# Kernel tuning notes

Measured on AMD Instinct MI355X. Metric: run time of the kernel, lower is better.

Reference implementation:

```python
import jax, jax.numpy as jnp
import numpy as np

WS = 8        # window_size
NH = 8        # num_heads
LN_EPS = 1e-5

# static relative-position index table [WS*WS, WS*WS], values in [0, (2*WS-1)**2)
def _rel_index(ws):
    coords = np.arange(ws)
    grid = np.stack(np.meshgrid(coords, coords, indexing='ij')).reshape(2, -1)  # [2, W2]
    rel = grid[:, :, None] - grid[:, None, :]            # [2, W2, W2]
    rel = rel.transpose(1, 2, 0).copy()                   # [W2, W2, 2]
    rel[..., 0] += ws - 1
    rel[..., 1] += ws - 1
    rel[..., 0] *= 2 * ws - 1
    return rel.sum(-1)                                    # [W2, W2]

REL_IDX = jnp.asarray(_rel_index(WS))


def _ln(x):
    # LayerNorm without affine params (elementwise_affine=False)
    mu = jnp.mean(x, axis=-1, keepdims=True)
    var = jnp.var(x, axis=-1, keepdims=True)
    return (x - mu) * jax.lax.rsqrt(var + LN_EPS)


def setup_inputs() -> dict:
    key = jax.random.key(0)
    ks = jax.random.split(key, 16)
    B, Hg, Wg, C = 8, 64, 64, 256
    L = Hg * Wg
    s = 0.02
    inp = {
        'x': jax.random.normal(ks[0], (B, L, C), jnp.float32),
        't_embed': jax.random.normal(ks[1], (B, C), jnp.float32),
        'H': Hg,
        'W': Wg,
        'adaln1_w': s * jax.random.normal(ks[2], (C, 2 * C), jnp.float32),
        'adaln1_b': jnp.zeros((2 * C,), jnp.float32),
        'adaln2_w': s * jax.random.normal(ks[3], (C, 2 * C), jnp.float32),
        'adaln2_b': jnp.zeros((2 * C,), jnp.float32),
        'bias_table': s * jax.random.normal(ks[4], ((2 * WS - 1) ** 2, NH), jnp.float32),
        'q_w': s * jax.random.normal(ks[5], (C, C), jnp.float32),
        'q_b': jnp.zeros((C,), jnp.float32),
        'k_w': s * jax.random.normal(ks[6], (C, C), jnp.float32),
        'k_b': jnp.zeros((C,), jnp.float32),
        'v_w': s * jax.random.normal(ks[7], (C, C), jnp.float32),
        'v_b': jnp.zeros((C,), jnp.float32),
        'o_w': s * jax.random.normal(ks[8], (C, C), jnp.float32),
        'o_b': jnp.zeros((C,), jnp.float32),
        'ffn1_w': s * jax.random.normal(ks[9], (C, 4 * C), jnp.float32),
        'ffn1_b': jnp.zeros((4 * C,), jnp.float32),
        'ffn2_w': s * jax.random.normal(ks[10], (4 * C, C), jnp.float32),
        'ffn2_b': jnp.zeros((C,), jnp.float32),
    }
    return inp


def reference(x, t_embed, H, W, adaln1_w, adaln1_b, adaln2_w, adaln2_b,
              bias_table, q_w, q_b, k_w, k_b, v_w, v_b, o_w, o_b,
              ffn1_w, ffn1_b, ffn2_w, ffn2_b):
    B, L, C = x.shape
    d = C // NH
    W2 = WS * WS
    sh = WS // 2  # cyclic shift (shifted=True)

    # --- AdaLN1 ---
    ss = t_embed @ adaln1_w + adaln1_b              # [B, 2C]
    scale, shift = jnp.split(ss, 2, axis=-1)
    xn = _ln(x) * (1.0 + scale[:, None, :]) + shift[:, None, :]

    # --- shifted window partition ---
    xg = xn.reshape(B, H, W, C)
    xg = jnp.roll(xg, (-sh, -sh), axis=(1, 2))
    xw = xg.reshape(B, H // WS, WS, W // WS, WS, C).transpose(0, 1, 3, 2, 4, 5)
    xw = xw.reshape(-1, W2, C)                       # [nwB, W2, C]
    nwB = xw.shape[0]

    # --- window attention with relative position bias ---
    q = (xw @ q_w + q_b).reshape(nwB, W2, NH, d).transpose(0, 2, 1, 3)
    k = (xw @ k_w + k_b).reshape(nwB, W2, NH, d).transpose(0, 2, 1, 3)
    v = (xw @ v_w + v_b).reshape(nwB, W2, NH, d).transpose(0, 2, 1, 3)
    logits = jnp.einsum('whqd,whkd->whqk', q, k) * (d ** -0.5)
    bias = bias_table[REL_IDX.reshape(-1)].reshape(W2, W2, NH).transpose(2, 0, 1)
    logits = logits + bias[None].astype(logits.dtype)
    attn = jax.nn.softmax(logits, axis=-1)
    out = jnp.einsum('whqk,whkd->whqd', attn, v).transpose(0, 2, 1, 3).reshape(nwB, W2, C)
    out = out @ o_w + o_b

    # --- window reverse + unshift ---
    xm = out.reshape(B, H // WS, W // WS, WS, WS, C).transpose(0, 1, 3, 2, 4, 5)
    xm = xm.reshape(B, H, W, C)
    xm = jnp.roll(xm, (sh, sh), axis=(1, 2))
    x = x + xm.reshape(B, L, C)

    # --- AdaLN2 + FFN (GELU exact, matching torch nn.GELU) ---
    ss2 = t_embed @ adaln2_w + adaln2_b
    sc2, sh2 = jnp.split(ss2, 2, axis=-1)
    xn2 = _ln(x) * (1.0 + sc2[:, None, :]) + sh2[:, None, :]
    h = jax.nn.gelu(xn2 @ ffn1_w + ffn1_b, approximate=False)
    x = x + (h @ ffn2_w + ffn2_b)
    return x
```

## Files before the change

### kernel.cpp

```cpp
#include <hip/hip_runtime.h>
#include <math.h>

#define WS_ 8
#define NH_ 8
#define C_ 256
#define B_ 8
#define M_ 32768
#define SH_ 4
#define LN_EPS 1e-5f
#define SL_ 8388608

typedef __attribute__((ext_vector_type(8))) short bf16x8;
typedef __attribute__((ext_vector_type(4))) float f32x4;

__device__ inline float b2f(unsigned short u) {
    union { unsigned int i; float f; } c; c.i = ((unsigned int)u) << 16; return c.f;
}
__device__ inline unsigned short f2b(float f) {
    union { unsigned int i; float f; } c; c.f = f;
    unsigned int u = c.i;
    return (unsigned short)((u + 0x7FFFu + ((u >> 16) & 1u)) >> 16);
}
__device__ inline float gelu_f(float x) {
    float t = 1.59576912160573f * (x + 0.044715f * x * x * x);
    return x / (1.f + __expf(-t));
}

__global__ void prep_k(const float* __restrict__ qw, const float* __restrict__ kw,
                       const float* __restrict__ vw, const float* __restrict__ ow,
                       const float* __restrict__ f1w, const float* __restrict__ f2w,
                       const float* __restrict__ qb, const float* __restrict__ kb,
                       const float* __restrict__ vb, const float* __restrict__ bt,
                       const float* __restrict__ te,
                       const float* __restrict__ a1w, const float* __restrict__ a1b,
                       const float* __restrict__ a2w, const float* __restrict__ a2b,
                       unsigned short* __restrict__ qkvT, unsigned short* __restrict__ oT,
                       unsigned short* __restrict__ f1T, unsigned short* __restrict__ f2T,
                       float* __restrict__ qkvB, float* __restrict__ bias_full,
                       float* __restrict__ ss1, float* __restrict__ ss2) {
    int t = blockIdx.x * 256 + threadIdx.x;
    if (t < 196608) {
        int n = t >> 8, k = t & 255;
        const float* w = n < 256 ? qw : (n < 512 ? kw : vw);
        qkvT[t] = f2b(w[k * 256 + (n & 255)]);
    } else if (t < 262144) {
        int i = t - 196608; int n = i >> 8, k = i & 255;
        oT[i] = f2b(ow[k * 256 + n]);
    } else if (t < 524288) {
        int i = t - 262144; int n = i >> 8, k = i & 255;
        f1T[i] = f2b(f1w[k * 1024 + n]);
    } else if (t < 786432) {
        int i = t - 524288; int n = i >> 10, k = i & 1023;
        f2T[i] = f2b(f2w[k * 256 + n]);
    } else if (t < 787200) {
        int i = t - 786432;
        qkvB[i] = i < 256 ? qb[i] : (i < 512 ? kb[i - 256] : vb[i - 512]);
    } else if (t < 819968) {
        int i = t - 787200;
        int head = i >> 12, qk = i & 4095;
        int q = qk >> 6, k = qk & 63;
        int qh = q >> 3, qw2 = q & 7, kh = k >> 3, kw2 = k & 7;
        bias_full[i] = bt[((qh - kh + 7) * 15 + (qw2 - kw2 + 7)) * 8 + head];
    } else if (t < 828160) {
        int i = t - 819968;
        int which = i >> 12;
        int rem = i & 4095;
        int b = rem >> 9, col = rem & 511;
        const float* w = which ? a2w : a1w;
        const float* bb = which ? a2b : a1b;
        const float* tr = te + b * C_;
        float acc = bb[col];
        for (int k = 0; k < C_; ++k) acc += tr[k] * w[k * 512 + col];
        (which ? ss2 : ss1)[b * 512 + col] = acc;
    }
}

__global__ __launch_bounds__(256) void ln_win_k(const float* __restrict__ x,
                                                const float* __restrict__ ss,
                                                unsigned short* __restrict__ xw) {
    int t = blockIdx.x * 4 + (threadIdx.x >> 6);
    int lane = threadIdx.x & 63;
    int b = t >> 12, rem = t & 4095;
    int hg = rem >> 6, wg = rem & 63;
    int hs = (hg + SH_) & 63, wsrc = (wg + SH_) & 63;
    size_t src = ((size_t)b << 12) + (hs << 6) + wsrc;
    float4 v = *(const float4*)&x[src * C_ + lane * 4];
    float s = v.x + v.y + v.z + v.w;
    float s2 = v.x * v.x + v.y * v.y + v.z * v.z + v.w * v.w;
#pragma unroll
    for (int m = 1; m < 64; m <<= 1) { s += __shfl_xor(s, m); s2 += __shfl_xor(s2, m); }
    float mu = s * (1.f / 256.f);
    float rstd = rsqrtf(s2 * (1.f / 256.f) - mu * mu + LN_EPS);
    float4 sc = *(const float4*)&ss[b * 512 + lane * 4];
    float4 sh = *(const float4*)&ss[b * 512 + 256 + lane * 4];
    int win = (b << 6) + ((hg >> 3) << 3) + (wg >> 3);
    int pos = ((hg & 7) << 3) + (wg & 7);
    ushort4 pk;
    pk.x = f2b((v.x - mu) * rstd * (1.f + sc.x) + sh.x);
    pk.y = f2b((v.y - mu) * rstd * (1.f + sc.y) + sh.y);
    pk.z = f2b((v.z - mu) * rstd * (1.f + sc.z) + sh.z);
    pk.w = f2b((v.w - mu) * rstd * (1.f + sc.w) + sh.w);
    *(ushort4*)(xw + (size_t)(win * 64 + pos) * C_ + lane * 4) = pk;
}

template <int KDIM, int MODE, int NT, int MINW>
__global__ __launch_bounds__(256, MINW) void gemm_bf16_k(
    const unsigned short* __restrict__ A, const unsigned short* __restrict__ Bt,
    const float* __restrict__ bias, const float* __restrict__ res,
    void* __restrict__ Cout, int Nout) {
    __shared__ __align__(16) unsigned short As[4][128 * 32];
    __shared__ __align__(16) unsigned short Bs[4][128 * 32];
    const int blk = blockIdx.x;
    const int xcd = blk & 7;
    const int idx = blk >> 3;
    const int mt = xcd + ((idx / NT) << 3);
    const int nt = idx % NT;
    const int bm = mt * 128, bn = nt * 128;
    const int tid = threadIdx.x;
    const int w = tid >> 6, lane = tid & 63;
    const int quad = lane >> 4, l16 = lane & 15;
    const int wm = (w >> 1) * 64, wn = (w & 1) * 64;
    const int srow = lane >> 2;
    const int qlog = ((lane & 3) ^ ((lane >> 3) & 3)) << 3;
    const int rsw = ((l16 >> 1) & 3) << 3;

    f32x4 acc[4][4] = {};

    for (int k0 = 0; k0 < KDIM; k0 += 128) {
        if (k0) __syncthreads();
#pragma unroll
        for (int h = 0; h < 4; ++h) {
#pragma unroll
            for (int j = 0; j < 2; ++j) {
                int r = j * 64 + w * 16 + srow;
                const unsigned short* ga = A + (size_t)(bm + r) * KDIM + k0 + h * 32 + qlog;
                unsigned short* la = &As[h][j * 2048 + w * 512 + lane * 8];
                __builtin_amdgcn_global_load_lds(
                    (const __attribute__((address_space(1))) void*)ga,
                    (__attribute__((address_space(3))) void*)la, 16, 0, 0);
                const unsigned short* gb = Bt + (size_t)(bn + r) * KDIM + k0 + h * 32 + qlog;
                unsigned short* lb = &Bs[h][j * 2048 + w * 512 + lane * 8];
                __builtin_amdgcn_global_load_lds(
                    (const __attribute__((address_space(1))) void*)gb,
                    (__attribute__((address_space(3))) void*)lb, 16, 0, 0);
            }
        }
        __syncthreads();
#pragma unroll
        for (int h = 0; h < 4; ++h) {
            bf16x8 af[4], bfr[4];
#pragma unroll
            for (int i = 0; i < 4; ++i)
                af[i] = *(const bf16x8*)&As[h][(wm + i * 16 + l16) * 32 + ((quad << 3) ^ rsw)];
#pragma unroll
            for (int j = 0; j < 4; ++j)
                bfr[j] = *(const bf16x8*)&Bs[h][(wn + j * 16 + l16) * 32 + ((quad << 3) ^ rsw)];
#pragma unroll
            for (int i = 0; i < 4; ++i)
#pragma unroll
                for (int j = 0; j < 4; ++j)
                    acc[i][j] = __builtin_amdgcn_mfma_f32_16x16x32_bf16(
                        bfr[j], af[i], acc[i][j], 0, 0, 0);
        }
    }

#pragma unroll
    for (int i = 0; i < 4; ++i) {
        const int row = bm + wm + i * 16 + l16;
        size_t rowbase = 0;
        if (MODE == 0) {
            int win = row >> 6, pos = row & 63;
            rowbase = (size_t)win * 16384 + pos * 32;
        } else {
            rowbase = (size_t)row * Nout;
        }
#pragma unroll
        for (int j = 0; j < 4; ++j) {
            const int col = bn + wn + j * 16 + quad * 4;
            float4 bv = *(const float4*)&bias[col];
            float v0 = acc[i][j][0] + bv.x, v1 = acc[i][j][1] + bv.y;
            float v2 = acc[i][j][2] + bv.z, v3 = acc[i][j][3] + bv.w;
            if (MODE == 0) {
                int which = col >> 8, head = (col >> 5) & 7, dc = col & 31;
                ushort4 pk = {f2b(v0), f2b(v1), f2b(v2), f2b(v3)};
                *(ushort4*)((unsigned short*)Cout + (size_t)which * SL_ + rowbase +
                            head * 2048 + dc) = pk;
            } else if (MODE == 2) {
                ushort4 pk = {f2b(gelu_f(v0)), f2b(gelu_f(v1)),
                              f2b(gelu_f(v2)), f2b(gelu_f(v3))};
                *(ushort4*)((unsigned short*)Cout + rowbase + col) = pk;
            } else {
                float4 rv = *(const float4*)&res[rowbase + col];
                float4 ov = {v0 + rv.x, v1 + rv.y, v2 + rv.z, v3 + rv.w};
                *(float4*)&((float*)Cout)[rowbase + col] = ov;
            }
        }
    }
}

__global__ __launch_bounds__(512, 2) void oproj_ln_k(
    const unsigned short* __restrict__ A, const unsigned short* __restrict__ Bt,
    const float* __restrict__ bias, const float* __restrict__ res,
    float* __restrict__ x1, const float* __restrict__ ss2,
    unsigned short* __restrict__ xn2) {
    __shared__ __align__(16) unsigned short As[4][128 * 32];
    __shared__ __align__(16) unsigned short Bs[4][256 * 32];
    const int bm = blockIdx.x * 128;
    const int tid = threadIdx.x;
    const int w = tid >> 6, lane = tid & 63;
    const int quad = lane >> 4, l16 = lane & 15;
    const int wrow = (w >> 2) * 64, wcol = (w & 3) * 64;
    const int rsw = ((l16 >> 1) & 3) << 3;
    const int srow = tid >> 2;
    const int gch = ((tid & 3) ^ ((srow >> 1) & 3)) << 3;

    f32x4 acc[4][4] = {};

    for (int k0 = 0; k0 < 256; k0 += 128) {
        if (k0) __syncthreads();
#pragma unroll
        for (int h = 0; h < 4; ++h) {
            const unsigned short* ga = A + (size_t)(bm + srow) * 256 + k0 + h * 32 + gch;
            __builtin_amdgcn_global_load_lds(
                (const __attribute__((address_space(1))) void*)ga,
                (__attribute__((address_space(3))) void*)&As[h][tid * 8], 16, 0, 0);
#pragma unroll
            for (int s = 0; s < 2; ++s) {
                const unsigned short* gb = Bt + (size_t)(s * 128 + srow) * 256 + k0 + h * 32 + gch;
                __builtin_amdgcn_global_load_lds(
                    (const __attribute__((address_space(1))) void*)gb,
                    (__attribute__((address_space(3))) void*)&Bs[h][s * 4096 + tid * 8], 16, 0, 0);
            }
        }
        __syncthreads();
#pragma unroll
        for (int h = 0; h < 4; ++h) {
            bf16x8 af[4], bfr[4];
#pragma unroll
            for (int i = 0; i < 4; ++i)
                af[i] = *(const bf16x8*)&As[h][(wrow + i * 16 + l16) * 32 + ((quad << 3) ^ rsw)];
#pragma unroll
            for (int j = 0; j < 4; ++j)
                bfr[j] = *(const bf16x8*)&Bs[h][(wcol + j * 16 + l16) * 32 + ((quad << 3) ^ rsw)];
#pragma unroll
            for (int i = 0; i < 4; ++i)
#pragma unroll
                for (int j = 0; j < 4; ++j)
                    acc[i][j] = __builtin_amdgcn_mfma_f32_16x16x32_bf16(
                        bfr[j], af[i], acc[i][j], 0, 0, 0);
        }
    }

    float ps[4], ps2[4];
#pragma unroll
    for (int i = 0; i < 4; ++i) {
        const int row = bm + wrow + i * 16 + l16;
        int win = row >> 6, pos = row & 63;
        int b = win >> 6, wh = (win >> 3) & 7, ww = win & 7;
        int hg = (wh << 3) + (pos >> 3), wg = (ww << 3) + (pos & 7);
        int hd = (hg + SH_) & 63, wd = (wg + SH_) & 63;
        size_t rowbase = (((size_t)b << 12) + (hd << 6) + wd) * C_;
        float s = 0.f, s2 = 0.f;
#pragma unroll
        for (int j = 0; j < 4; ++j) {
            const int col = wcol + j * 16 + quad * 4;
            float4 bv = *(const float4*)&bias[col];
            float4 rv = *(const float4*)&res[rowbase + col];
            float4 ov = {acc[i][j][0] + bv.x + rv.x, acc[i][j][1] + bv.y + rv.y,
                         acc[i][j][2] + bv.z + rv.z, acc[i][j][3] + bv.w + rv.w};
            *(float4*)&x1[rowbase + col] = ov;
            acc[i][j][0] = ov.x; acc[i][j][1] = ov.y;
            acc[i][j][2] = ov.z; acc[i][j][3] = ov.w;
            s += ov.x + ov.y + ov.z + ov.w;
            s2 += ov.x * ov.x + ov.y * ov.y + ov.z * ov.z + ov.w * ov.w;
        }
        ps[i] = s; ps2[i] = s2;
    }
#pragma unroll
    for (int i = 0; i < 4; ++i) {
        ps[i] += __shfl_xor(ps[i], 16);  ps[i] += __shfl_xor(ps[i], 32);
        ps2[i] += __shfl_xor(ps2[i], 16); ps2[i] += __shfl_xor(ps2[i], 32);
    }
    float* sred = (float*)&As[0][0];
    __syncthreads();
    if (quad == 0) {
#pragma unroll
        for (int i = 0; i < 4; ++i) {
            int r = i * 16 + l16;
            sred[(w * 64 + r) * 2 + 0] = ps[i];
            sred[(w * 64 + r) * 2 + 1] = ps2[i];
        }
    }
    __syncthreads();
#pragma unroll
    for (int i = 0; i < 4; ++i) {
        int r = i * 16 + l16;
        float s = 0.f, s2 = 0.f;
#pragma unroll
        for (int cw = 0; cw < 4; ++cw) {
            s  += sred[(((w >> 2) * 4 + cw) * 64 + r) * 2 + 0];
            s2 += sred[(((w >> 2) * 4 + cw) * 64 + r) * 2 + 1];
        }
        float mu = s * (1.f / 256.f);
        float rstd = rsqrtf(s2 * (1.f / 256.f) - mu * mu + LN_EPS);
        const int row = bm + wrow + i * 16 + l16;
        int win = row >> 6, pos = row & 63;
        int b = win >> 6, wh = (win >> 3) & 7, ww = win & 7;
        int hg = (wh << 3) + (pos >> 3), wg = (ww << 3) + (pos & 7);
        int hd = (hg + SH_) & 63, wd = (wg + SH_) & 63;
        size_t rowbase = (((size_t)b << 12) + (hd << 6) + wd) * C_;
#pragma unroll
        for (int j = 0; j < 4; ++j) {
            const int col = wcol + j * 16 + quad * 4;
            float4 scv = *(const float4*)&ss2[b * 512 + col];
            float4 shv = *(const float4*)&ss2[b * 512 + 256 + col];
            ushort4 pk;
            pk.x = f2b((acc[i][j][0] - mu) * rstd * (1.f + scv.x) + shv.x);
            pk.y = f2b((acc[i][j][1] - mu) * rstd * (1.f + scv.y) + shv.y);
            pk.z = f2b((acc[i][j][2] - mu) * rstd * (1.f + scv.z) + shv.z);
            pk.w = f2b((acc[i][j][3] - mu) * rstd * (1.f + scv.w) + shv.w);
            *(ushort4*)(xn2 + rowbase + col) = pk;
        }
    }
}

__global__ __launch_bounds__(256) void attn_mfma_k(
    const unsigned short* __restrict__ qkv, const float* __restrict__ bias_full,
    unsigned short* __restrict__ attn_out) {
    __shared__ __align__(16) unsigned short Pb[4][64 * 66];
    __shared__ __align__(16) unsigned short Vt[4][32 * 66];
    const int w = threadIdx.x >> 6, lane = threadIdx.x & 63;
    const int wh = blockIdx.x * 4 + w;
    const int win = wh >> 3, head = wh & 7;
    const int quad = lane >> 4, l16 = lane & 15;

    const unsigned short* qp = qkv + (size_t)win * 16384 + head * 2048;
    const unsigned short* kp = qp + SL_;
    const unsigned short* vp = qp + 2 * (size_t)SL_;

    {
        const uint4* v4 = (const uint4*)(vp + lane * 32);
        unsigned short* dst = &Vt[w][0];
#pragma unroll
        for (int c = 0; c < 4; ++c) {
            uint4 u = v4[c];
            unsigned int uu[4] = {u.x, u.y, u.z, u.w};
#pragma unroll
            for (int p = 0; p < 4; ++p) {
                int d0 = c * 8 + p * 2;
                dst[d0 * 66 + lane] = (unsigned short)(uu[p] & 0xffff);
                dst[(d0 + 1) * 66 + lane] = (unsigned short)(uu[p] >> 16);
            }
        }
    }

    bf16x8 qf[4], kf[4];
#pragma unroll
    for (int i = 0; i < 4; ++i) {
        qf[i] = *(const bf16x8*)(qp + (i * 16 + l16) * 32 + quad * 8);
        kf[i] = *(const bf16x8*)(kp + (i * 16 + l16) * 32 + quad * 8);
    }

    f32x4 s[4][4] = {};
#pragma unroll
    for (int i = 0; i < 4; ++i)
#pragma unroll
        for (int j = 0; j < 4; ++j)
            s[i][j] = __builtin_amdgcn_mfma_f32_16x16x32_bf16(qf[i], kf[j], s[i][j], 0, 0, 0);

    const float scale = 0.17677669529663687f;
    const float* bf = bias_full + head * 4096;
    float rs[4][4];
#pragma unroll
    for (int i = 0; i < 4; ++i) {
#pragma unroll
        for (int r = 0; r < 4; ++r) {
            int row = i * 16 + quad * 4 + r;
            float acc = 0.f;
#pragma unroll
            for (int j = 0; j < 4; ++j) {
                float e = __expf(s[i][j][r] * scale + bf[row * 64 + j * 16 + l16]);
                s[i][j][r] = e;
                acc += e;
            }
#pragma unroll
            for (int msk = 1; msk < 16; msk <<= 1) acc += __shfl_xor(acc, msk);
            rs[i][r] = 1.f / acc;
        }
    }

#pragma unroll
    for (int i = 0; i < 4; ++i)
#pragma unroll
        for (int j = 0; j < 4; ++j)
#pragma unroll
            for (int r = 0; r < 4; ++r)
                Pb[w][(i * 16 + quad * 4 + r) * 66 + j * 16 + l16] = f2b(s[i][j][r]);

    __syncthreads();

    f32x4 o[4][2] = {};
#pragma unroll
    for (int st = 0; st < 2; ++st) {
        bf16x8 bv[2];
#pragma unroll
        for (int jo = 0; jo < 2; ++jo)
            bv[jo] = *(const bf16x8*)&Vt[w][(jo * 16 + l16) * 66 + st * 32 + quad * 8];
#pragma unroll
        for (int i = 0; i < 4; ++i) {
            bf16x8 af = *(const bf16x8*)&Pb[w][(i * 16 + l16) * 66 + st * 32 + quad * 8];
#pragma unroll
            for (int jo = 0; jo < 2; ++jo)
                o[i][jo] = __builtin_amdgcn_mfma_f32_16x16x32_bf16(af, bv[jo], o[i][jo], 0, 0, 0);
        }
    }

#pragma unroll
    for (int i = 0; i < 4; ++i)
#pragma unroll
        for (int jo = 0; jo < 2; ++jo)
#pragma unroll
            for (int r = 0; r < 4; ++r) {
                int row = i * 16 + quad * 4 + r;
                int d = jo * 16 + l16;
                attn_out[((size_t)(win * 64 + row)) * C_ + head * 32 + d] =
                    f2b(o[i][jo][r] * rs[i][r]);
            }
}

extern "C" void kernel_launch(void* const* d_in, const int* in_sizes, int n_in,
                              void* d_out, int out_size, void* d_ws, size_t ws_size,
                              hipStream_t stream) {
    const float* x        = (const float*)d_in[0];
    const float* t_embed  = (const float*)d_in[1];
    const float* adaln1_w = (const float*)d_in[4];
    const float* adaln1_b = (const float*)d_in[5];
    const float* adaln2_w = (const float*)d_in[6];
    const float* adaln2_b = (const float*)d_in[7];
    const float* bt       = (const float*)d_in[8];
    const float* q_w = (const float*)d_in[9],  *q_b = (const float*)d_in[10];
    const float* k_w = (const float*)d_in[11], *k_b = (const float*)d_in[12];
    const float* v_w = (const float*)d_in[13], *v_b = (const float*)d_in[14];
    const float* o_w = (const float*)d_in[15], *o_b = (const float*)d_in[16];
    const float* f1_w = (const float*)d_in[17], *f1_b = (const float*)d_in[18];
    const float* f2_w = (const float*)d_in[19], *f2_b = (const float*)d_in[20];
    float* out = (float*)d_out;

    char* wsb = (char*)d_ws;
    float* ss1            = (float*)(wsb + 0);
    float* ss2            = (float*)(wsb + 16384);
    float* qkvB           = (float*)(wsb + 32768);
    unsigned short* qkvT  = (unsigned short*)(wsb + 36864);
    unsigned short* oT    = (unsigned short*)(wsb + 430080);
    unsigned short* f1T   = (unsigned short*)(wsb + 561152);
    unsigned short* f2T   = (unsigned short*)(wsb + 1085440);
    float* bias_full      = (float*)(wsb + 1609728);
    unsigned short* xw    = (unsigned short*)(wsb + 2097152);
    unsigned short* qkv   = (unsigned short*)(wsb + 18874368);
    unsigned short* attn  = (unsigned short*)(wsb + 69206016);
    unsigned short* xn2   = xw;
    unsigned short* hbuf  = qkv;
    float* x1             = (float*)(wsb + 85983232);

    prep_k<<<3235, 256, 0, stream>>>(q_w, k_w, v_w, o_w, f1_w, f2_w, q_b, k_b, v_b, bt,
                                     t_embed, adaln1_w, adaln1_b, adaln2_w, adaln2_b,
                                     qkvT, oT, f1T, f2T, qkvB, bias_full, ss1, ss2);
    ln_win_k<<<8192, 256, 0, stream>>>(x, ss1, xw);

    gemm_bf16_k<256, 0, 6, 2><<<1536, 256, 0, stream>>>(xw, qkvT, qkvB, nullptr, qkv, 768);

    attn_mfma_k<<<1024, 256, 0, stream>>>(qkv, bias_full, attn);

    oproj_ln_k<<<256, 512, 0, stream>>>(attn, oT, o_b, x, x1, ss2, xn2);

    gemm_bf16_k<256, 2, 8, 2><<<2048, 256, 0, stream>>>(xn2, f1T, f1_b, nullptr, hbuf, 1024);
    gemm_bf16_k<1024, 3, 2, 2><<<512, 256, 0, stream>>>(hbuf, f2T, f2_b, x1, out, 256);
}
```

Measured before the change: 270.8 us.

## Halve GEMM K-step LDS footprint and stage bf16 epilogue through swizzled LDS

The generic bf16 GEMM now loads 64-wide K chunks instead of 128, halving shared memory to 32KB so more blocks can be resident. Launch-bound minimum waves change to 3 for the QKV and FFN1 GEMMs and to 1 for FFN2. For the bf16-output modes (QKV scatter and GELU), the epilogue writes results into swizzled LDS and then emits full 16-byte row-contiguous stores instead of scattered 8-byte stores. The cost is twice as many barriers in the K loop and an extra LDS round trip in the epilogue.

```diff
diff --git a/kernel.cpp b/kernel.cpp
--- a/kernel.cpp
+++ b/kernel.cpp
@@ -108,8 +108,9 @@
     const unsigned short* __restrict__ A, const unsigned short* __restrict__ Bt,
     const float* __restrict__ bias, const float* __restrict__ res,
     void* __restrict__ Cout, int Nout) {
-    __shared__ __align__(16) unsigned short As[4][128 * 32];
-    __shared__ __align__(16) unsigned short Bs[4][128 * 32];
+    __shared__ __align__(16) unsigned short smem[16384];
+    unsigned short (*As)[4096] = (unsigned short (*)[4096])&smem[0];
+    unsigned short (*Bs)[4096] = (unsigned short (*)[4096])&smem[8192];
     const int blk = blockIdx.x;
     const int xcd = blk & 7;
     const int idx = blk >> 3;
@@ -126,10 +127,10 @@
 
     f32x4 acc[4][4] = {};
 
-    for (int k0 = 0; k0 < KDIM; k0 += 128) {
+    for (int k0 = 0; k0 < KDIM; k0 += 64) {
         if (k0) __syncthreads();
 #pragma unroll
-        for (int h = 0; h < 4; ++h) {
+        for (int h = 0; h < 2; ++h) {
 #pragma unroll
             for (int j = 0; j < 2; ++j) {
                 int r = j * 64 + w * 16 + srow;
@@ -147,7 +148,7 @@
         }
         __syncthreads();
 #pragma unroll
-        for (int h = 0; h < 4; ++h) {
+        for (int h = 0; h < 2; ++h) {
             bf16x8 af[4], bfr[4];
 #pragma unroll
             for (int i = 0; i < 4; ++i)
@@ -164,32 +165,56 @@
         }
     }
 
-#pragma unroll
-    for (int i = 0; i < 4; ++i) {
-        const int row = bm + wm + i * 16 + l16;
-        size_t rowbase = 0;
-        if (MODE == 0) {
-            int win = row >> 6, pos = row & 63;
-            rowbase = (size_t)win * 16384 + pos * 32;
-        } else {
-            rowbase = (size_t)row * Nout;
-        }
-#pragma unroll
-        for (int j = 0; j < 4; ++j) {
-            const int col = bn + wn + j * 16 + quad * 4;
-            float4 bv = *(const float4*)&bias[col];
-            float v0 = acc[i][j][0] + bv.x, v1 = acc[i][j][1] + bv.y;
-            float v2 = acc[i][j][2] + bv.z, v3 = acc[i][j][3] + bv.w;
-            if (MODE == 0) {
+    if constexpr (MODE == 0 || MODE == 2) {
+        __syncthreads();
+#pragma unroll
+        for (int i = 0; i < 4; ++i) {
+            const int lrow = wm + i * 16 + l16;
+#pragma unroll
+            for (int j = 0; j < 4; ++j) {
+                const int lcol = wn + j * 16 + quad * 4;
+                float4 bv = *(const float4*)&bias[bn + lcol];
+                float v0 = acc[i][j][0] + bv.x, v1 = acc[i][j][1] + bv.y;
+                float v2 = acc[i][j][2] + bv.z, v3 = acc[i][j][3] + bv.w;
+                ushort4 pk;
+                if (MODE == 2) {
+                    pk.x = f2b(gelu_f(v0)); pk.y = f2b(gelu_f(v1));
+                    pk.z = f2b(gelu_f(v2)); pk.w = f2b(gelu_f(v3));
+                } else {
+                    pk.x = f2b(v0); pk.y = f2b(v1); pk.z = f2b(v2); pk.w = f2b(v3);
+                }
+                int sw = (lcol >> 3) ^ (lrow & 7);
+                *(ushort4*)&smem[lrow * 128 + sw * 8 + (lcol & 7)] = pk;
+            }
+        }
+        __syncthreads();
+#pragma unroll
+        for (int p = 0; p < 8; ++p) {
+            const int lrow = p * 16 + (tid >> 4);
+            const int c16 = tid & 15;
+            bf16x8 v = *(const bf16x8*)&smem[lrow * 128 + ((c16 ^ (lrow & 7)) * 8)];
+            const int grow = bm + lrow;
+            if (MODE == 2) {
+                *(bf16x8*)((unsigned short*)Cout + (size_t)grow * Nout + bn + c16 * 8) = v;
+            } else {
+                int win = grow >> 6, pos = grow & 63;
+                int col = bn + c16 * 8;
                 int which = col >> 8, head = (col >> 5) & 7, dc = col & 31;
-                ushort4 pk = {f2b(v0), f2b(v1), f2b(v2), f2b(v3)};
-                *(ushort4*)((unsigned short*)Cout + (size_t)which * SL_ + rowbase +
-                            head * 2048 + dc) = pk;
-            } else if (MODE == 2) {
-                ushort4 pk = {f2b(gelu_f(v0)), f2b(gelu_f(v1)),
-                              f2b(gelu_f(v2)), f2b(gelu_f(v3))};
-                *(ushort4*)((unsigned short*)Cout + rowbase + col) = pk;
-            } else {
+                *(bf16x8*)((unsigned short*)Cout + (size_t)which * SL_ +
+                           (size_t)win * 16384 + pos * 32 + head * 2048 + dc) = v;
+            }
+        }
+    } else {
+#pragma unroll
+        for (int i = 0; i < 4; ++i) {
+            const int row = bm + wm + i * 16 + l16;
+            size_t rowbase = (size_t)row * Nout;
+#pragma unroll
+            for (int j = 0; j < 4; ++j) {
+                const int col = bn + wn + j * 16 + quad * 4;
+                float4 bv = *(const float4*)&bias[col];
+                float v0 = acc[i][j][0] + bv.x, v1 = acc[i][j][1] + bv.y;
+                float v2 = acc[i][j][2] + bv.z, v3 = acc[i][j][3] + bv.w;
                 float4 rv = *(const float4*)&res[rowbase + col];
                 float4 ov = {v0 + rv.x, v1 + rv.y, v2 + rv.z, v3 + rv.w};
                 *(float4*)&((float*)Cout)[rowbase + col] = ov;
@@ -467,12 +492,12 @@
                                      qkvT, oT, f1T, f2T, qkvB, bias_full, ss1, ss2);
     ln_win_k<<<8192, 256, 0, stream>>>(x, ss1, xw);
 
-    gemm_bf16_k<256, 0, 6, 2><<<1536, 256, 0, stream>>>(xw, qkvT, qkvB, nullptr, qkv, 768);
+    gemm_bf16_k<256, 0, 6, 3><<<1536, 256, 0, stream>>>(xw, qkvT, qkvB, nullptr, qkv, 768);
 
     attn_mfma_k<<<1024, 256, 0, stream>>>(qkv, bias_full, attn);
 
     oproj_ln_k<<<256, 512, 0, stream>>>(attn, oT, o_b, x, x1, ss2, xn2);
 
-    gemm_bf16_k<256, 2, 8, 2><<<2048, 256, 0, stream>>>(xn2, f1T, f1_b, nullptr, hbuf, 1024);
-    gemm_bf16_k<1024, 3, 2, 2><<<512, 256, 0, stream>>>(hbuf, f2T, f2_b, x1, out, 256);
-}
+    gemm_bf16_k<256, 2, 8, 3><<<2048, 256, 0, stream>>>(xn2, f1T, f1_b, nullptr, hbuf, 1024);
+    gemm_bf16_k<1024, 3, 2, 1><<<512, 256, 0, stream>>>(hbuf, f2T, f2_b, x1, out, 256);
+}
```

Result: faster. 261.9 us (-3.3%).
